# Optimization experiments

Hardware: AMD Instinct MI355X
Metric: run time of the kernel (lower is better)

## Reference

```python
import jax, jax.numpy as jnp
from jax import lax
import numpy as np

D_MODEL = 1024
D_STATE = 64
D_CONV = 4
EXPAND = 2
HEADDIM = 64
D_INNER = EXPAND * D_MODEL          # 2048
NHEADS = D_INNER // HEADDIM         # 32
CHUNK = 64
CONV_DIM = D_INNER + 2 * D_STATE    # 2176
D_IN_PROJ = 2 * D_INNER + 2 * D_STATE + NHEADS  # 4256
B_SZ = 4
SEQLEN = 2048
EPS = 1e-5


def _silu(x):
    return x * jax.nn.sigmoid(x)


def _segsum(x):
    # x: [..., T]; returns [..., T, T] with [i,j] = sum_{j<k<=i} x[k], -inf above diag
    T = x.shape[-1]
    xe = jnp.broadcast_to(x[..., None], x.shape + (T,))
    strict_lower = jnp.tril(jnp.ones((T, T), bool), -1)
    xe = jnp.where(strict_lower, xe, 0.0)
    s = jnp.cumsum(xe, axis=-2)
    lower = jnp.tril(jnp.ones((T, T), bool), 0)
    return jnp.where(lower, s, -jnp.inf)


def setup_inputs() -> dict:
    key = jax.random.key(0)
    ks = jax.random.split(key, 5)
    u = jax.random.normal(ks[0], (B_SZ, SEQLEN, D_MODEL), jnp.float32)
    W_in = jax.random.normal(ks[1], (D_IN_PROJ, D_MODEL), jnp.float32) * 0.02
    conv_w = jax.random.normal(ks[2], (CONV_DIM, 1, D_CONV), jnp.float32) * 0.2  # depthwise kernel
    conv_b = jnp.zeros((CONV_DIM,), jnp.float32)
    dt_bias = jax.random.uniform(ks[3], (NHEADS,), jnp.float32, -1.0, 1.0)
    A_log = jnp.log(jnp.linspace(1.0, float(NHEADS), NHEADS)).astype(jnp.float32)
    D = jnp.ones((NHEADS,), jnp.float32)
    norm_w = jnp.ones((D_INNER,), jnp.float32)
    W_out = jax.random.normal(ks[4], (D_MODEL, D_INNER), jnp.float32) * 0.02
    return dict(u=u, W_in=W_in, conv_w=conv_w, conv_b=conv_b, dt_bias=dt_bias,
                A_log=A_log, D=D, norm_w=norm_w, W_out=W_out)


def reference(u, W_in, conv_w, conv_b, dt_bias, A_log, D, norm_w, W_out):
    b, s, _ = u.shape
    A = -jnp.exp(A_log)                                   # [H]
    zxbcdt = u @ W_in.T                                   # [b,s,D_IN_PROJ]
    z = zxbcdt[..., :D_INNER]
    xBC = zxbcdt[..., D_INNER:D_INNER + CONV_DIM]
    dt = jax.nn.softplus(zxbcdt[..., D_INNER + CONV_DIM:] + dt_bias)  # [b,s,H]

    # causal depthwise conv1d (left pad d_conv-1 == torch pad-both + slice[:s])
    xc = lax.conv_general_dilated(
        xBC.transpose(0, 2, 1), conv_w, window_strides=(1,),
        padding=[(D_CONV - 1, 0)], feature_group_count=CONV_DIM,
        dimension_numbers=('NCH', 'OIH', 'NCH'))
    xBC = _silu(xc.transpose(0, 2, 1) + conv_b)           # [b,s,CONV_DIM]

    x = xBC[..., :D_INNER].reshape(b, s, NHEADS, HEADDIM)
    Bm = xBC[..., D_INNER:D_INNER + D_STATE]              # [b,s,N]
    Cm = xBC[..., D_INNER + D_STATE:]                     # [b,s,N]

    # SSD chunked scan
    nch = s // CHUNK
    xs = (x * dt[..., None]).reshape(b, nch, CHUNK, NHEADS, HEADDIM)
    Ad = (A * dt).reshape(b, nch, CHUNK, NHEADS)
    Br = Bm.reshape(b, nch, CHUNK, D_STATE)
    Cr = Cm.reshape(b, nch, CHUNK, D_STATE)
    A_ch = Ad.transpose(0, 1, 3, 2)                       # [b,c,h,l]
    A_cum = jnp.cumsum(A_ch, axis=-1)
    L = jnp.exp(_segsum(A_ch))                            # [b,c,h,l,l]
    Y_diag = jnp.einsum('bcln,bcsn,bchls,bcshp->bclhp', Cr, Br, L, xs)
    decay_states = jnp.exp(A_cum[..., -1:] - A_cum)       # [b,c,h,l]
    states = jnp.einsum('bchl,bcln,bclhp->bchpn', decay_states, Br, xs)
    init = jnp.zeros((b, 1, NHEADS, HEADDIM, D_STATE), xs.dtype)
    states = jnp.concatenate([init, states], axis=1)      # [b,c+1,h,p,n]
    total_decay = jnp.pad(A_cum[..., -1].transpose(0, 2, 1), ((0, 0), (0, 0), (1, 0)))
    decay_chunk = jnp.exp(_segsum(total_decay))           # [b,h,c+1,c+1]
    new_states = jnp.einsum('bhzc,bchpn->bzhpn', decay_chunk, states)
    states = new_states[:, :-1]                           # [b,c,h,p,n]
    state_decay_out = jnp.exp(A_cum)
    Y_off = jnp.einsum('bcln,bchpn,bchl->bclhp', Cr, states, state_decay_out)
    y = (Y_diag + Y_off).reshape(b, s, NHEADS, HEADDIM)

    y = y + x * D[:, None]
    y = y.reshape(b, s, D_INNER)
    # gated RMSNorm
    y = y * _silu(z)
    y = y * lax.rsqrt(jnp.mean(y * y, axis=-1, keepdims=True) + EPS) * norm_w
    return y @ W_out.T
```

## Files before the change

### kernel.cpp

```cpp
#include <hip/hip_runtime.h>
#include <hip/hip_bf16.h>

#define BSZ 4
#define SEQ 2048
#define DMODEL 1024
#define DINNER 2048
#define DSTATE 64
#define NH 32
#define HD 64
#define CKL 64
#define NCH 32
#define CONVD 2176
#define DPROJ 4256
#define N1 4224
#define MTOT 8192
#define YSTR 72

typedef __hip_bfloat16 bf16;
typedef __attribute__((ext_vector_type(8))) short short8;
typedef __attribute__((ext_vector_type(4))) short short4_;
typedef __attribute__((ext_vector_type(4))) float f32x4;

__device__ __forceinline__ float sigmoidf_(float x) { return 1.0f / (1.0f + __expf(-x)); }
__device__ __forceinline__ float bits2f(short s) { return __uint_as_float(((unsigned)(unsigned short)s) << 16); }
__device__ __forceinline__ short f2bits(float f) {
    bf16 h = __float2bfloat16(f);
    return *reinterpret_cast<short*>(&h);
}

__device__ __forceinline__ void gl_lds16(const bf16* g, bf16* l) {
    __builtin_amdgcn_global_load_lds((const __attribute__((address_space(1))) void*)g,
                                     (__attribute__((address_space(3))) void*)l, 16, 0, 0);
}

__device__ __forceinline__ void store_val(float* p, float v) { *p = v; }
__device__ __forceinline__ void store_val(bf16* p, float v) { *p = __float2bfloat16(v); }

__global__ void k_cvt(const float* __restrict__ src, bf16* __restrict__ dst, int n) {
    int i = blockIdx.x * 256 + threadIdx.x;
    int g = i * 4;
    if (g < n) {
        f32x4 f = *(const f32x4*)&src[g];
        short4_ o;
#pragma unroll
        for (int j = 0; j < 4; j++) o[j] = f2bits(f[j]);
        *(short4_*)&dst[g] = o;
    }
}

template <typename TOUT>
__global__ __launch_bounds__(256) void k_gemm_bt(const bf16* __restrict__ A, const bf16* __restrict__ W,
                                                 TOUT* __restrict__ C, int N, int K) {
    __shared__ __align__(16) bf16 lA[128 * 64];
    __shared__ __align__(16) bf16 lB[128 * 64];
    const int tid = threadIdx.x;
    const int lane = tid & 63, w = tid >> 6;
    const int wm = w >> 1, wn = w & 1;
    const int lr = lane & 15, lk = lane >> 4;
    const int m0 = blockIdx.y * 128, n0 = blockIdx.x * 128;

    f32x4 acc[4][4];
#pragma unroll
    for (int i = 0; i < 4; i++)
#pragma unroll
        for (int j = 0; j < 4; j++) acc[i][j] = (f32x4){0.f, 0.f, 0.f, 0.f};

    const int r = tid >> 3;
    const int cs = ((tid & 7) ^ (r & 7)) * 8;
    const bf16* ga = A + (size_t)(m0 + r) * K + cs;
    const bf16* gb = W + (size_t)(n0 + r) * K + cs;
    bf16* la0 = lA + tid * 8;
    bf16* lb0 = lB + tid * 8;
    const int sx = (lr & 7);

    for (int kt = 0; kt < K; kt += 64) {
#pragma unroll
        for (int i = 0; i < 4; i++) {
            gl_lds16(ga + kt + (size_t)(32 * i) * K, la0 + 2048 * i);
            gl_lds16(gb + kt + (size_t)(32 * i) * K, lb0 + 2048 * i);
        }
        __syncthreads();
#pragma unroll
        for (int hh = 0; hh < 2; hh++) {
            const int cb = ((lk + 4 * hh) ^ sx) * 8;
            short8 af[4], bfr[4];
#pragma unroll
            for (int im = 0; im < 4; im++)
                af[im] = *(const short8*)&lA[(wm * 64 + im * 16 + lr) * 64 + cb];
#pragma unroll
            for (int jn = 0; jn < 4; jn++)
                bfr[jn] = *(const short8*)&lB[(wn * 64 + jn * 16 + lr) * 64 + cb];
#pragma unroll
            for (int im = 0; im < 4; im++)
#pragma unroll
                for (int jn = 0; jn < 4; jn++)
                    acc[im][jn] = __builtin_amdgcn_mfma_f32_16x16x32_bf16(af[im], bfr[jn], acc[im][jn], 0, 0, 0);
        }
        __syncthreads();
    }
#pragma unroll
    for (int im = 0; im < 4; im++) {
        int row = m0 + wm * 64 + im * 16 + lk * 4;
#pragma unroll
        for (int jn = 0; jn < 4; jn++) {
            int col = n0 + wn * 64 + jn * 16 + lr;
            TOUT* cp = C + (size_t)row * N + col;
#pragma unroll
            for (int rr = 0; rr < 4; rr++) store_val(cp + (size_t)rr * N, acc[im][jn][rr]);
        }
    }
}

__global__ __launch_bounds__(256) void k_prep(const float* __restrict__ u, const float* __restrict__ W_in,
                                              const float* __restrict__ dt_bias,
                                              bf16* __restrict__ u_b, float* __restrict__ dtt) {
    __shared__ __align__(16) float us[8 * DMODEL];
    const int t0 = blockIdx.x * 8;
    const int tid = threadIdx.x;
    const float* ur = u + (size_t)t0 * DMODEL;
    bf16* ub = u_b + (size_t)t0 * DMODEL;
#pragma unroll
    for (int i = 0; i < 8; i++) {
        int idx = (i * 256 + tid) * 4;
        f32x4 v = *(const f32x4*)&ur[idx];
        *(f32x4*)&us[idx] = v;
        short4_ o;
#pragma unroll
        for (int j = 0; j < 4; j++) o[j] = f2bits(v[j]);
        *(short4_*)&ub[idx] = o;
    }
    __syncthreads();
    const int h = tid >> 3, sub = tid & 7;
    const float* wr = W_in + (size_t)(DPROJ - NH + h) * DMODEL;
    float s[8] = {};
    for (int k = sub * 4; k < DMODEL; k += 32) {
        f32x4 w4 = *(const f32x4*)&wr[k];
#pragma unroll
        for (int rr = 0; rr < 8; rr++) {
            const float* up = &us[rr * DMODEL + k];
            s[rr] += up[0] * w4[0] + up[1] * w4[1] + up[2] * w4[2] + up[3] * w4[3];
        }
    }
#pragma unroll
    for (int rr = 0; rr < 8; rr++) {
        s[rr] += __shfl_down(s[rr], 4, 8);
        s[rr] += __shfl_down(s[rr], 2, 8);
        s[rr] += __shfl_down(s[rr], 1, 8);
    }
    if (sub == 0) {
        float bh = dt_bias[h];
#pragma unroll
        for (int rr = 0; rr < 8; rr++) {
            float x = s[rr] + bh;
            dtt[(size_t)h * MTOT + t0 + rr] = (x > 20.f) ? x : log1pf(__expf(x));
        }
    }
}

__global__ void k_conv(const bf16* __restrict__ zx, const float* __restrict__ cw,
                       const float* __restrict__ cb, bf16* __restrict__ xbc) {
    int i = blockIdx.x * 256 + threadIdx.x;
    int g = i * 4;
    if (g >= MTOT * CONVD) return;
    int c0 = g % CONVD;
    int t = g / CONVD;
    int s = t & (SEQ - 1);
    const short* base = (const short*)(zx + (size_t)t * N1 + DINNER + c0);
    f32x4 w0 = *(const f32x4*)&cw[(c0 + 0) * 4];
    f32x4 w1 = *(const f32x4*)&cw[(c0 + 1) * 4];
    f32x4 w2 = *(const f32x4*)&cw[(c0 + 2) * 4];
    f32x4 w3 = *(const f32x4*)&cw[(c0 + 3) * 4];
    f32x4 a = *(const f32x4*)&cb[c0];
#pragma unroll
    for (int k = 0; k < 4; k++) {
        int st = s - 3 + k;
        if (st >= 0) {
            short4_ v = *(const short4_*)(base + (long)(k - 3) * N1);
            a[0] += bits2f(v[0]) * w0[k];
            a[1] += bits2f(v[1]) * w1[k];
            a[2] += bits2f(v[2]) * w2[k];
            a[3] += bits2f(v[3]) * w3[k];
        }
    }
    short4_ o;
#pragma unroll
    for (int j = 0; j < 4; j++) o[j] = f2bits(a[j] * sigmoidf_(a[j]));
    *(short4_*)&xbc[g] = o;
}

__global__ __launch_bounds__(256) void k_ssd(const bf16* __restrict__ xbc, const float* __restrict__ dtt,
                                             const float* __restrict__ A_log, const float* __restrict__ Dp,
                                             bf16* __restrict__ zx) {
    __shared__ __align__(16) short Ct[64 * YSTR];
    __shared__ __align__(16) short Bt[64 * YSTR];
    __shared__ __align__(16) short Bn[64 * YSTR];
    __shared__ __align__(16) short Xt[32 * YSTR];
    __shared__ __align__(16) short Xd[32 * YSTR];
    __shared__ __align__(16) short Sb[32 * YSTR];
    __shared__ __align__(16) short Gs[4 * 16 * YSTR];
    __shared__ __align__(16) float Sf[32 * 68];
    __shared__ float sdt2[2][64], sAc2[2][64], sf2[2][64], set2[2];

    const int ph = blockIdx.x, h = blockIdx.y, b = blockIdx.z;
    const int tid = threadIdx.x;
    const int lane = tid & 63, w = tid >> 6;
    const int lr = lane & 15, lk = lane >> 4;
    const float Ah = -__expf(A_log[h]);
    const float Dh = Dp[h];
    const int xcol = h * HD + ph * 32;

    const int lrow = tid >> 2, c0 = (tid & 3) * 16, px = (tid & 3) * 8;
    const int zl = 16 * w + (lane >> 2), zp = (lane & 3) * 8;

    short8 rC0, rC1, rB0, rB1, rX, rZ;
    float rdt;
    auto load_chunk = [&](int cc) {
        int rows0 = b * SEQ + cc * CKL;
        const short* rp = (const short*)(xbc + (size_t)(rows0 + lrow) * CONVD);
        rC0 = *(const short8*)&rp[DINNER + DSTATE + c0];
        rC1 = *(const short8*)&rp[DINNER + DSTATE + c0 + 8];
        rB0 = *(const short8*)&rp[DINNER + c0];
        rB1 = *(const short8*)&rp[DINNER + c0 + 8];
        rX  = *(const short8*)&rp[xcol + px];
        rZ  = *(const short8*)((const short*)zx + (size_t)(rows0 + zl) * N1 + xcol + zp);
        rdt = dtt[(size_t)h * MTOT + rows0 + lane];
    };

    for (int i = tid; i < 32 * 68; i += 256) Sf[i] = 0.f;
    load_chunk(0);
    if (tid < 64) {
        float dv = rdt;
        float v = Ah * dv;
#pragma unroll
        for (int d = 1; d < 64; d <<= 1) { float o = __shfl_up(v, d); if (tid >= d) v += o; }
        float tot = __shfl(v, 63);
        sdt2[0][tid] = dv; sAc2[0][tid] = v; sf2[0][tid] = __expf(tot - v) * dv;
        if (tid == 63) set2[0] = __expf(tot);
    }
    __syncthreads();

    for (int c = 0; c < NCH; c++) {
        const int par = c & 1;
        const int rows0 = b * SEQ + c * CKL;
        *(short8*)&Ct[lrow * YSTR + c0] = rC0;
        *(short8*)&Ct[lrow * YSTR + c0 + 8] = rC1;
        *(short8*)&Bt[lrow * YSTR + c0] = rB0;
        *(short8*)&Bt[lrow * YSTR + c0 + 8] = rB1;
#pragma unroll
        for (int j = 0; j < 8; j++) {
            Bn[(c0 + j) * YSTR + lrow] = rB0[j];
            Bn[(c0 + 8 + j) * YSTR + lrow] = rB1[j];
        }
        float sfl = sf2[par][lrow];
#pragma unroll
        for (int j = 0; j < 8; j++) {
            Xt[(px + j) * YSTR + lrow] = rX[j];
            Xd[(px + j) * YSTR + lrow] = f2bits(bits2f(rX[j]) * sfl);
        }
        {
            int sp = tid >> 3, sn = (tid & 7) * 8;
            f32x4 a0 = *(const f32x4*)&Sf[sp * 68 + sn];
            f32x4 a1 = *(const f32x4*)&Sf[sp * 68 + sn + 4];
            short8 o;
#pragma unroll
            for (int j = 0; j < 4; j++) { o[j] = f2bits(a0[j]); o[4 + j] = f2bits(a1[j]); }
            *(short8*)&Sb[sp * YSTR + sn] = o;
        }
        __syncthreads();

        float etot = set2[par];
        short8 zcur = rZ;
        if (c + 1 < NCH) load_chunk(c + 1);

        short8 cf0 = *(const short8*)&Ct[(16 * w + lr) * YSTR + lk * 8];
        short8 cf1 = *(const short8*)&Ct[(16 * w + lr) * YSTR + 32 + lk * 8];
        f32x4 acc[2];
#pragma unroll
        for (int t = 0; t < 2; t++) {
            short8 s0 = *(const short8*)&Sb[(16 * t + lr) * YSTR + lk * 8];
            short8 s1 = *(const short8*)&Sb[(16 * t + lr) * YSTR + 32 + lk * 8];
            acc[t] = __builtin_amdgcn_mfma_f32_16x16x32_bf16(cf0, s0, (f32x4){0.f, 0.f, 0.f, 0.f}, 0, 0, 0);
            acc[t] = __builtin_amdgcn_mfma_f32_16x16x32_bf16(cf1, s1, acc[t], 0, 0, 0);
        }
        float sAcl[4], el[4];
#pragma unroll
        for (int rr = 0; rr < 4; rr++) { sAcl[rr] = sAc2[par][16 * w + lk * 4 + rr]; el[rr] = __expf(sAcl[rr]); }
#pragma unroll
        for (int t = 0; t < 2; t++)
#pragma unroll
            for (int rr = 0; rr < 4; rr++) acc[t][rr] *= el[rr];
        short* gw = Gs + w * 16 * YSTR;
#pragma unroll
        for (int t = 0; t < 4; t++) {
            short8 b0 = *(const short8*)&Bt[(16 * t + lr) * YSTR + lk * 8];
            short8 b1 = *(const short8*)&Bt[(16 * t + lr) * YSTR + 32 + lk * 8];
            f32x4 g = __builtin_amdgcn_mfma_f32_16x16x32_bf16(cf0, b0, (f32x4){0.f, 0.f, 0.f, 0.f}, 0, 0, 0);
            g = __builtin_amdgcn_mfma_f32_16x16x32_bf16(cf1, b1, g, 0, 0, 0);
            int s = 16 * t + lr;
            float sAcs = sAc2[par][s], dts = sdt2[par][s];
#pragma unroll
            for (int rr = 0; rr < 4; rr++) {
                int l = 16 * w + lk * 4 + rr;
                float v = (s <= l) ? g[rr] * __expf(sAcl[rr] - sAcs) * dts : 0.f;
                gw[(lk * 4 + rr) * YSTR + s] = f2bits(v);
            }
        }
        short8 gf0 = *(const short8*)&gw[lr * YSTR + lk * 8];
        short8 gf1 = *(const short8*)&gw[lr * YSTR + 32 + lk * 8];
#pragma unroll
        for (int t = 0; t < 2; t++) {
            short8 x0 = *(const short8*)&Xt[(16 * t + lr) * YSTR + lk * 8];
            short8 x1 = *(const short8*)&Xt[(16 * t + lr) * YSTR + 32 + lk * 8];
            acc[t] = __builtin_amdgcn_mfma_f32_16x16x32_bf16(gf0, x0, acc[t], 0, 0, 0);
            acc[t] = __builtin_amdgcn_mfma_f32_16x16x32_bf16(gf1, x1, acc[t], 0, 0, 0);
        }
        {
            int pw = w & 1, nh2 = w >> 1;
            short8 xd0 = *(const short8*)&Xd[(16 * pw + lr) * YSTR + lk * 8];
            short8 xd1 = *(const short8*)&Xd[(16 * pw + lr) * YSTR + 32 + lk * 8];
#pragma unroll
            for (int j = 0; j < 2; j++) {
                int nt = 2 * nh2 + j;
                short8 b0 = *(const short8*)&Bn[(16 * nt + lr) * YSTR + lk * 8];
                short8 b1 = *(const short8*)&Bn[(16 * nt + lr) * YSTR + 32 + lk * 8];
                f32x4 sacc = __builtin_amdgcn_mfma_f32_16x16x32_bf16(xd0, b0, (f32x4){0.f, 0.f, 0.f, 0.f}, 0, 0, 0);
                sacc = __builtin_amdgcn_mfma_f32_16x16x32_bf16(xd1, b1, sacc, 0, 0, 0);
#pragma unroll
                for (int rr = 0; rr < 4; rr++) {
                    int n = 16 * nt + lr;
                    int p = 16 * pw + lk * 4 + rr;
                    Sf[p * 68 + n] = Sf[p * 68 + n] * etot + sacc[rr];
                }
            }
        }
#pragma unroll
        for (int t = 0; t < 2; t++) {
#pragma unroll
            for (int rr = 0; rr < 4; rr++) {
                int p = 16 * t + lr;
                int l = 16 * w + lk * 4 + rr;
                float y = acc[t][rr] + Dh * bits2f(Xt[p * YSTR + l]);
                Ct[l * YSTR + p] = f2bits(y);
            }
        }
        {
            short8 y8 = *(const short8*)&Ct[zl * YSTR + zp];
            short* zpp = (short*)zx + (size_t)(rows0 + zl) * N1 + xcol + zp;
            short8 o;
#pragma unroll
            for (int j = 0; j < 8; j++) {
                float z = bits2f(zcur[j]);
                o[j] = f2bits(bits2f(y8[j]) * (z * sigmoidf_(z)));
            }
            *(short8*)zpp = o;
        }
        if (c + 1 < NCH && tid < 64) {
            int p2 = (c + 1) & 1;
            float dv = rdt;
            float v = Ah * dv;
#pragma unroll
            for (int d = 1; d < 64; d <<= 1) { float o = __shfl_up(v, d); if (tid >= d) v += o; }
            float tot = __shfl(v, 63);
            sdt2[p2][tid] = dv; sAc2[p2][tid] = v; sf2[p2][tid] = __expf(tot - v) * dv;
            if (tid == 63) set2[p2] = __expf(tot);
        }
        __syncthreads();
    }
}

__global__ __launch_bounds__(256) void k_norm(const bf16* __restrict__ zx, const float* __restrict__ nw,
                                              bf16* __restrict__ yb) {
    __shared__ float red[4];
    int t = blockIdx.x, tid = threadIdx.x;
    const short* row = (const short*)(zx + (size_t)t * N1);
    short8 v8 = *(const short8*)&row[tid * 8];
    float v[8];
    float ss = 0.f;
#pragma unroll
    for (int i = 0; i < 8; i++) {
        v[i] = bits2f(v8[i]);
        ss += v[i] * v[i];
    }
#pragma unroll
    for (int d = 32; d > 0; d >>= 1) ss += __shfl_down(ss, d);
    if ((tid & 63) == 0) red[tid >> 6] = ss;
    __syncthreads();
    float scale = rsqrtf((red[0] + red[1] + red[2] + red[3]) * (1.0f / DINNER) + 1e-5f);
    f32x4 w0 = *(const f32x4*)&nw[tid * 8];
    f32x4 w1 = *(const f32x4*)&nw[tid * 8 + 4];
    short8 o;
#pragma unroll
    for (int i = 0; i < 4; i++) o[i] = f2bits(v[i] * scale * w0[i]);
#pragma unroll
    for (int i = 0; i < 4; i++) o[4 + i] = f2bits(v[4 + i] * scale * w1[i]);
    *(short8*)&((short*)yb)[(size_t)t * DINNER + tid * 8] = o;
}

extern "C" void kernel_launch(void* const* d_in, const int* in_sizes, int n_in,
                              void* d_out, int out_size, void* d_ws, size_t ws_size,
                              hipStream_t stream) {
    const float* u       = (const float*)d_in[0];
    const float* W_in    = (const float*)d_in[1];
    const float* conv_w  = (const float*)d_in[2];
    const float* conv_b  = (const float*)d_in[3];
    const float* dt_bias = (const float*)d_in[4];
    const float* A_log   = (const float*)d_in[5];
    const float* Dp      = (const float*)d_in[6];
    const float* norm_w  = (const float*)d_in[7];
    const float* W_out   = (const float*)d_in[8];
    float* out = (float*)d_out;

    char* ws = (char*)d_ws;
    bf16* zx     = (bf16*)ws;  ws += (size_t)MTOT * N1 * 2;
    bf16* xbc    = (bf16*)ws;  ws += (size_t)MTOT * CONVD * 2;
    bf16* wout_b = (bf16*)ws;  ws += (size_t)DMODEL * DINNER * 2;
    float* dtt   = (float*)ws; ws += (size_t)NH * MTOT * 4;
    bf16* y_b    = (bf16*)xbc;

    bf16* u_b   = (bf16*)d_out;
    bf16* win_b = (bf16*)((char*)d_out + (size_t)MTOT * DMODEL * 2);

    k_prep<<<MTOT / 8, 256, 0, stream>>>(u, W_in, dt_bias, u_b, dtt);
    k_cvt<<<(N1 * DMODEL / 4 + 255) / 256, 256, 0, stream>>>(W_in, win_b, N1 * DMODEL);
    k_cvt<<<(DMODEL * DINNER / 4 + 255) / 256, 256, 0, stream>>>(W_out, wout_b, DMODEL * DINNER);

    k_gemm_bt<bf16><<<dim3(N1 / 128, MTOT / 128), 256, 0, stream>>>(u_b, win_b, zx, N1, DMODEL);

    k_conv<<<(MTOT * CONVD / 4 + 255) / 256, 256, 0, stream>>>(zx, conv_w, conv_b, xbc);

    k_ssd<<<dim3(2, NH, BSZ), 256, 0, stream>>>(xbc, dtt, A_log, Dp, zx);

    k_norm<<<MTOT, 256, 0, stream>>>(zx, norm_w, y_b);

    k_gemm_bt<float><<<dim3(DMODEL / 128, MTOT / 128), 256, 0, stream>>>(y_b, wout_b, out, DMODEL, DINNER);
}
```

Before: 401.9 us.

## Fold RMSNorm into output GEMM via per-row scale and weight-prescaled W_out

```diff
diff --git a/kernel.cpp b/kernel.cpp
--- a/kernel.cpp
+++ b/kernel.cpp
@@ -33,12 +33,8 @@
                                      (__attribute__((address_space(3))) void*)l, 16, 0, 0);
 }
 
-__device__ __forceinline__ void store_val(float* p, float v) { *p = v; }
-__device__ __forceinline__ void store_val(bf16* p, float v) { *p = __float2bfloat16(v); }
-
 __global__ void k_cvt(const float* __restrict__ src, bf16* __restrict__ dst, int n) {
-    int i = blockIdx.x * 256 + threadIdx.x;
-    int g = i * 4;
+    int g = (blockIdx.x * 256 + threadIdx.x) * 4;
     if (g < n) {
         f32x4 f = *(const f32x4*)&src[g];
         short4_ o;
@@ -48,9 +44,21 @@
     }
 }
 
-template <typename TOUT>
+__global__ void k_cvtw(const float* __restrict__ src, const float* __restrict__ nw,
+                       bf16* __restrict__ dst, int n) {
+    int g = (blockIdx.x * 256 + threadIdx.x) * 4;
+    if (g < n) {
+        f32x4 f = *(const f32x4*)&src[g];
+        f32x4 w = *(const f32x4*)&nw[g & (DINNER - 1)];
+        short4_ o;
+#pragma unroll
+        for (int j = 0; j < 4; j++) o[j] = f2bits(f[j] * w[j]);
+        *(short4_*)&dst[g] = o;
+    }
+}
+
 __global__ __launch_bounds__(256) void k_gemm_bt(const bf16* __restrict__ A, const bf16* __restrict__ W,
-                                                 TOUT* __restrict__ C, int N, int K) {
+                                                 bf16* __restrict__ C, int N, int K, int lda) {
     __shared__ __align__(16) bf16 lA[128 * 64];
     __shared__ __align__(16) bf16 lB[128 * 64];
     const int tid = threadIdx.x;
@@ -67,7 +75,7 @@
 
     const int r = tid >> 3;
     const int cs = ((tid & 7) ^ (r & 7)) * 8;
-    const bf16* ga = A + (size_t)(m0 + r) * K + cs;
+    const bf16* ga = A + (size_t)(m0 + r) * lda + cs;
     const bf16* gb = W + (size_t)(n0 + r) * K + cs;
     bf16* la0 = lA + tid * 8;
     bf16* lb0 = lB + tid * 8;
@@ -76,7 +84,7 @@
     for (int kt = 0; kt < K; kt += 64) {
 #pragma unroll
         for (int i = 0; i < 4; i++) {
-            gl_lds16(ga + kt + (size_t)(32 * i) * K, la0 + 2048 * i);
+            gl_lds16(ga + kt + (size_t)(32 * i) * lda, la0 + 2048 * i);
             gl_lds16(gb + kt + (size_t)(32 * i) * K, lb0 + 2048 * i);
         }
         __syncthreads();
@@ -104,11 +112,92 @@
 #pragma unroll
         for (int jn = 0; jn < 4; jn++) {
             int col = n0 + wn * 64 + jn * 16 + lr;
-            TOUT* cp = C + (size_t)row * N + col;
-#pragma unroll
-            for (int rr = 0; rr < 4; rr++) store_val(cp + (size_t)rr * N, acc[im][jn][rr]);
-        }
-    }
+            bf16* cp = C + (size_t)row * N + col;
+#pragma unroll
+            for (int rr = 0; rr < 4; rr++) cp[(size_t)rr * N] = __float2bfloat16(acc[im][jn][rr]);
+        }
+    }
+}
+
+__global__ __launch_bounds__(256) void k_gemm2(const bf16* __restrict__ A, const bf16* __restrict__ W,
+                                               const float* __restrict__ rs, float* __restrict__ C) {
+    __shared__ __align__(16) bf16 lA[128 * 64];
+    __shared__ __align__(16) bf16 lB[64 * 64];
+    const int tid = threadIdx.x;
+    const int lane = tid & 63, w = tid >> 6;
+    const int lr = lane & 15, lk = lane >> 4;
+    const int m0 = blockIdx.y * 128, n0 = blockIdx.x * 64;
+    const int K = DINNER, N = DMODEL;
+
+    f32x4 acc[2][4];
+#pragma unroll
+    for (int i = 0; i < 2; i++)
+#pragma unroll
+        for (int j = 0; j < 4; j++) acc[i][j] = (f32x4){0.f, 0.f, 0.f, 0.f};
+
+    const int r = tid >> 3;
+    const int cs = ((tid & 7) ^ (r & 7)) * 8;
+    const bf16* ga = A + (size_t)(m0 + r) * N1 + cs;
+    const bf16* gb = W + (size_t)(n0 + r) * K + cs;
+    bf16* la0 = lA + tid * 8;
+    bf16* lb0 = lB + tid * 8;
+    const int sx = (lr & 7);
+
+    for (int kt = 0; kt < K; kt += 64) {
+#pragma unroll
+        for (int i = 0; i < 4; i++)
+            gl_lds16(ga + kt + (size_t)(32 * i) * N1, la0 + 2048 * i);
+#pragma unroll
+        for (int i = 0; i < 2; i++)
+            gl_lds16(gb + kt + (size_t)(32 * i) * K, lb0 + 2048 * i);
+        __syncthreads();
+#pragma unroll
+        for (int hh = 0; hh < 2; hh++) {
+            const int cb = ((lk + 4 * hh) ^ sx) * 8;
+            short8 af[2], bfr[4];
+#pragma unroll
+            for (int im = 0; im < 2; im++)
+                af[im] = *(const short8*)&lA[(w * 32 + im * 16 + lr) * 64 + cb];
+#pragma unroll
+            for (int jn = 0; jn < 4; jn++)
+                bfr[jn] = *(const short8*)&lB[(jn * 16 + lr) * 64 + cb];
+#pragma unroll
+            for (int im = 0; im < 2; im++)
+#pragma unroll
+                for (int jn = 0; jn < 4; jn++)
+                    acc[im][jn] = __builtin_amdgcn_mfma_f32_16x16x32_bf16(af[im], bfr[jn], acc[im][jn], 0, 0, 0);
+        }
+        __syncthreads();
+    }
+#pragma unroll
+    for (int im = 0; im < 2; im++) {
+        int row = m0 + w * 32 + im * 16 + lk * 4;
+#pragma unroll
+        for (int rr = 0; rr < 4; rr++) {
+            float s = rs[row + rr];
+#pragma unroll
+            for (int jn = 0; jn < 4; jn++) {
+                int col = n0 + jn * 16 + lr;
+                C[(size_t)(row + rr) * N + col] = acc[im][jn][rr] * s;
+            }
+        }
+    }
+}
+
+__global__ __launch_bounds__(256) void k_rms(const bf16* __restrict__ zx, float* __restrict__ rs) {
+    __shared__ float red[4];
+    int t = blockIdx.x, tid = threadIdx.x;
+    const short* row = (const short*)(zx + (size_t)t * N1);
+    short8 v8 = *(const short8*)&row[tid * 8];
+    float ss = 0.f;
+#pragma unroll
+    for (int i = 0; i < 8; i++) { float v = bits2f(v8[i]); ss += v * v; }
+#pragma unroll
+    for (int d = 32; d > 0; d >>= 1) ss += __shfl_down(ss, d);
+    if ((tid & 63) == 0) red[tid >> 6] = ss;
+    __syncthreads();
+    if (tid == 0)
+        rs[t] = rsqrtf((red[0] + red[1] + red[2] + red[3]) * (1.0f / DINNER) + 1e-5f);
 }
 
 __global__ __launch_bounds__(256) void k_prep(const float* __restrict__ u, const float* __restrict__ W_in,
@@ -159,8 +248,7 @@
 
 __global__ void k_conv(const bf16* __restrict__ zx, const float* __restrict__ cw,
                        const float* __restrict__ cb, bf16* __restrict__ xbc) {
-    int i = blockIdx.x * 256 + threadIdx.x;
-    int g = i * 4;
+    int g = (blockIdx.x * 256 + threadIdx.x) * 4;
     if (g >= MTOT * CONVD) return;
     int c0 = g % CONVD;
     int t = g / CONVD;
@@ -195,11 +283,11 @@
     __shared__ __align__(16) short Bt[64 * YSTR];
     __shared__ __align__(16) short Bn[64 * YSTR];
     __shared__ __align__(16) short Xt[32 * YSTR];
-    __shared__ __align__(16) short Xd[32 * YSTR];
     __shared__ __align__(16) short Sb[32 * YSTR];
     __shared__ __align__(16) short Gs[4 * 16 * YSTR];
     __shared__ __align__(16) float Sf[32 * 68];
-    __shared__ float sdt2[2][64], sAc2[2][64], sf2[2][64], set2[2];
+    __shared__ __align__(16) float sdt2[2][64], sAc2[2][64], sf2[2][64];
+    __shared__ float set2[2];
 
     const int ph = blockIdx.x, h = blockIdx.y, b = blockIdx.z;
     const int tid = threadIdx.x;
@@ -250,12 +338,7 @@
         for (int j = 0; j < 8; j++) {
             Bn[(c0 + j) * YSTR + lrow] = rB0[j];
             Bn[(c0 + 8 + j) * YSTR + lrow] = rB1[j];
-        }
-        float sfl = sf2[par][lrow];
-#pragma unroll
-        for (int j = 0; j < 8; j++) {
             Xt[(px + j) * YSTR + lrow] = rX[j];
-            Xd[(px + j) * YSTR + lrow] = f2bits(bits2f(rX[j]) * sfl);
         }
         {
             int sp = tid >> 3, sn = (tid & 7) * 8;
@@ -316,8 +399,20 @@
         }
         {
             int pw = w & 1, nh2 = w >> 1;
-            short8 xd0 = *(const short8*)&Xd[(16 * pw + lr) * YSTR + lk * 8];
-            short8 xd1 = *(const short8*)&Xd[(16 * pw + lr) * YSTR + 32 + lk * 8];
+            short8 xt0 = *(const short8*)&Xt[(16 * pw + lr) * YSTR + lk * 8];
+            short8 xt1 = *(const short8*)&Xt[(16 * pw + lr) * YSTR + 32 + lk * 8];
+            f32x4 sa0 = *(const f32x4*)&sf2[par][lk * 8];
+            f32x4 sa1 = *(const f32x4*)&sf2[par][lk * 8 + 4];
+            f32x4 sb0 = *(const f32x4*)&sf2[par][32 + lk * 8];
+            f32x4 sb1 = *(const f32x4*)&sf2[par][32 + lk * 8 + 4];
+            short8 xd0, xd1;
+#pragma unroll
+            for (int j = 0; j < 4; j++) {
+                xd0[j]     = f2bits(bits2f(xt0[j])     * sa0[j]);
+                xd0[4 + j] = f2bits(bits2f(xt0[4 + j]) * sa1[j]);
+                xd1[j]     = f2bits(bits2f(xt1[j])     * sb0[j]);
+                xd1[4 + j] = f2bits(bits2f(xt1[4 + j]) * sb1[j]);
+            }
 #pragma unroll
             for (int j = 0; j < 2; j++) {
                 int nt = 2 * nh2 + j;
@@ -366,34 +461,6 @@
         }
         __syncthreads();
     }
-}
-
-__global__ __launch_bounds__(256) void k_norm(const bf16* __restrict__ zx, const float* __restrict__ nw,
-                                              bf16* __restrict__ yb) {
-    __shared__ float red[4];
-    int t = blockIdx.x, tid = threadIdx.x;
-    const short* row = (const short*)(zx + (size_t)t * N1);
-    short8 v8 = *(const short8*)&row[tid * 8];
-    float v[8];
-    float ss = 0.f;
-#pragma unroll
-    for (int i = 0; i < 8; i++) {
-        v[i] = bits2f(v8[i]);
-        ss += v[i] * v[i];
-    }
-#pragma unroll
-    for (int d = 32; d > 0; d >>= 1) ss += __shfl_down(ss, d);
-    if ((tid & 63) == 0) red[tid >> 6] = ss;
-    __syncthreads();
-    float scale = rsqrtf((red[0] + red[1] + red[2] + red[3]) * (1.0f / DINNER) + 1e-5f);
-    f32x4 w0 = *(const f32x4*)&nw[tid * 8];
-    f32x4 w1 = *(const f32x4*)&nw[tid * 8 + 4];
-    short8 o;
-#pragma unroll
-    for (int i = 0; i < 4; i++) o[i] = f2bits(v[i] * scale * w0[i]);
-#pragma unroll
-    for (int i = 0; i < 4; i++) o[4 + i] = f2bits(v[4 + i] * scale * w1[i]);
-    *(short8*)&((short*)yb)[(size_t)t * DINNER + tid * 8] = o;
 }
 
 extern "C" void kernel_launch(void* const* d_in, const int* in_sizes, int n_in,
@@ -415,22 +482,22 @@
     bf16* xbc    = (bf16*)ws;  ws += (size_t)MTOT * CONVD * 2;
     bf16* wout_b = (bf16*)ws;  ws += (size_t)DMODEL * DINNER * 2;
     float* dtt   = (float*)ws; ws += (size_t)NH * MTOT * 4;
-    bf16* y_b    = (bf16*)xbc;
+    float* rsb   = (float*)ws; ws += (size_t)MTOT * 4;
 
     bf16* u_b   = (bf16*)d_out;
     bf16* win_b = (bf16*)((char*)d_out + (size_t)MTOT * DMODEL * 2);
 
     k_prep<<<MTOT / 8, 256, 0, stream>>>(u, W_in, dt_bias, u_b, dtt);
     k_cvt<<<(N1 * DMODEL / 4 + 255) / 256, 256, 0, stream>>>(W_in, win_b, N1 * DMODEL);
-    k_cvt<<<(DMODEL * DINNER / 4 + 255) / 256, 256, 0, stream>>>(W_out, wout_b, DMODEL * DINNER);
-
-    k_gemm_bt<bf16><<<dim3(N1 / 128, MTOT / 128), 256, 0, stream>>>(u_b, win_b, zx, N1, DMODEL);
+    k_cvtw<<<(DMODEL * DINNER / 4 + 255) / 256, 256, 0, stream>>>(W_out, norm_w, wout_b, DMODEL * DINNER);
+
+    k_gemm_bt<<<dim3(N1 / 128, MTOT / 128), 256, 0, stream>>>(u_b, win_b, zx, N1, DMODEL, DMODEL);
 
     k_conv<<<(MTOT * CONVD / 4 + 255) / 256, 256, 0, stream>>>(zx, conv_w, conv_b, xbc);
 
     k_ssd<<<dim3(2, NH, BSZ), 256, 0, stream>>>(xbc, dtt, A_log, Dp, zx);
 
-    k_norm<<<MTOT, 256, 0, stream>>>(zx, norm_w, y_b);
-
-    k_gemm_bt<float><<<dim3(DMODEL / 128, MTOT / 128), 256, 0, stream>>>(y_b, wout_b, out, DMODEL, DINNER);
-}
+    k_rms<<<MTOT, 256, 0, stream>>>(zx, rsb);
+
+    k_gemm2<<<dim3(DMODEL / 64, MTOT / 128), 256, 0, stream>>>(zx, wout_b, rsb, out);
+}
```

Result: no change. 405.8 us (+1.0%).
